# Kernel optimization log

Measured on AMD Instinct MI355X. Metric: run time of the kernel, lower is better.

## Reference

```python
import jax, jax.numpy as jnp
import numpy as np

J = 16384
D = 2048

def setup_inputs() -> dict:
    key = jax.random.key(0)
    embeddings = jax.random.normal(key, (J, D), dtype=jnp.float32)
    return {"embeddings": embeddings}

def reference(embeddings) -> jnp.ndarray:
    J_, d = embeddings.shape
    # position indices j=1..J, feature indices k=1..d (as in the torch loop)
    j = jnp.arange(1, J_ + 1, dtype=embeddings.dtype)  # [J]
    k = jnp.arange(1, d + 1, dtype=embeddings.dtype)   # [d]
    a = 1.0 - j / J_            # [J]
    b = 1.0 - 2.0 * j / J_      # [J]
    # L[j,k] = (1 - j/J) - (k/d)*(1 - 2j/J)
    L = a[:, None] - (k / d)[None, :] * b[:, None]  # [J, d]
    return jnp.sum(L * embeddings, axis=0)  # [d]
```

## Files before the change

kernel.cpp:

```cpp
#include <hip/hip_runtime.h>


constexpr int D_COLS = 2048;
constexpr int J_ROWS = 16384;
constexpr int T1 = 512;
constexpr int B1_MAX = 512;

__global__ __launch_bounds__(T1) void pe_stage1(const float* __restrict__ E,
                                                float* __restrict__ ws,
                                                int nb) {
    const int tid  = threadIdx.x;
    const int col0 = tid * 4;
    const float invJ = 1.0f / (float)J_ROWS;
    const float invD = 1.0f / (float)D_COLS;
    const float c0 = (float)(col0 + 1) * invD;
    const float c1 = (float)(col0 + 2) * invD;
    const float c2 = (float)(col0 + 3) * invD;
    const float c3 = (float)(col0 + 4) * invD;

    float4 acc = make_float4(0.f, 0.f, 0.f, 0.f);
    for (int row = blockIdx.x; row < J_ROWS; row += nb) {
        const float jf = (float)(row + 1);
        const float a = fmaf(-jf,        invJ, 1.0f);
        const float b = fmaf(-2.0f * jf, invJ, 1.0f);
        const float4 e = *reinterpret_cast<const float4*>(E + (size_t)row * D_COLS + col0);
        acc.x = fmaf(fmaf(-c0, b, a), e.x, acc.x);
        acc.y = fmaf(fmaf(-c1, b, a), e.y, acc.y);
        acc.z = fmaf(fmaf(-c2, b, a), e.z, acc.z);
        acc.w = fmaf(fmaf(-c3, b, a), e.w, acc.w);
    }
    *reinterpret_cast<float4*>(ws + (size_t)blockIdx.x * D_COLS + col0) = acc;
}

__global__ __launch_bounds__(256) void pe_stage2(const float* __restrict__ ws,
                                                 float* __restrict__ out,
                                                 int nb) {
    const int k = blockIdx.x * 256 + threadIdx.x;
    if (k >= D_COLS) return;
    float s0 = 0.f, s1 = 0.f, s2 = 0.f, s3 = 0.f;
    int b = 0;
    for (; b + 3 < nb; b += 4) {
        s0 += ws[(size_t)(b + 0) * D_COLS + k];
        s1 += ws[(size_t)(b + 1) * D_COLS + k];
        s2 += ws[(size_t)(b + 2) * D_COLS + k];
        s3 += ws[(size_t)(b + 3) * D_COLS + k];
    }
    for (; b < nb; ++b) s0 += ws[(size_t)b * D_COLS + k];
    out[k] = (s0 + s1) + (s2 + s3);
}

extern "C" void kernel_launch(void* const* d_in, const int* in_sizes, int n_in,
                              void* d_out, int out_size, void* d_ws, size_t ws_size,
                              hipStream_t stream) {
    const float* E = (const float*)d_in[0];
    float* out = (float*)d_out;
    float* ws = (float*)d_ws;

    int nb = B1_MAX;
    const size_t per_block = (size_t)D_COLS * sizeof(float);
    if (ws_size < (size_t)nb * per_block) {
        nb = (int)(ws_size / per_block);
        if (nb < 1) nb = 1;
    }

    pe_stage1<<<nb, T1, 0, stream>>>(E, ws, nb);
    pe_stage2<<<(D_COLS + 255) / 256, 256, 0, stream>>>(ws, out, nb);
}
```

Measured before the change: 225.8 us.

## Replace two-stage reduction with atomic accumulation and unroll row loop by two

The workspace write plus second reduction kernel is replaced by float atomicAdd of each block's partial sums straight into the output, with a small zeroing kernel launched first. The row loop now issues two independent row loads per iteration to raise memory-level parallelism. This removes the 4 MB workspace round trip and the stage-2 pass, at the cost of contended atomics (512 per column) and a summation order that varies from run to run.

```diff
diff --git a/kernel.cpp b/kernel.cpp
--- a/kernel.cpp
+++ b/kernel.cpp
@@ -4,11 +4,15 @@
 constexpr int D_COLS = 2048;
 constexpr int J_ROWS = 16384;
 constexpr int T1 = 512;
-constexpr int B1_MAX = 512;
+constexpr int NB = 512;
 
-__global__ __launch_bounds__(T1) void pe_stage1(const float* __restrict__ E,
-                                                float* __restrict__ ws,
-                                                int nb) {
+__global__ __launch_bounds__(T1) void pe_zero(float* __restrict__ out) {
+    *reinterpret_cast<float4*>(out + threadIdx.x * 4) =
+        make_float4(0.f, 0.f, 0.f, 0.f);
+}
+
+__global__ __launch_bounds__(T1) void pe_fused(const float* __restrict__ E,
+                                               float* __restrict__ out) {
     const int tid  = threadIdx.x;
     const int col0 = tid * 4;
     const float invJ = 1.0f / (float)J_ROWS;
@@ -19,34 +23,33 @@
     const float c3 = (float)(col0 + 4) * invD;
 
     float4 acc = make_float4(0.f, 0.f, 0.f, 0.f);
-    for (int row = blockIdx.x; row < J_ROWS; row += nb) {
-        const float jf = (float)(row + 1);
-        const float a = fmaf(-jf,        invJ, 1.0f);
-        const float b = fmaf(-2.0f * jf, invJ, 1.0f);
-        const float4 e = *reinterpret_cast<const float4*>(E + (size_t)row * D_COLS + col0);
-        acc.x = fmaf(fmaf(-c0, b, a), e.x, acc.x);
-        acc.y = fmaf(fmaf(-c1, b, a), e.y, acc.y);
-        acc.z = fmaf(fmaf(-c2, b, a), e.z, acc.z);
-        acc.w = fmaf(fmaf(-c3, b, a), e.w, acc.w);
+    for (int row = blockIdx.x; row < J_ROWS; row += 2 * NB) {
+        const int r0 = row;
+        const int r1 = row + NB;
+        const float4 e0 = *reinterpret_cast<const float4*>(E + (size_t)r0 * D_COLS + col0);
+        const float4 e1 = *reinterpret_cast<const float4*>(E + (size_t)r1 * D_COLS + col0);
+
+        const float j0 = (float)(r0 + 1);
+        const float a0 = fmaf(-j0,        invJ, 1.0f);
+        const float b0 = fmaf(-2.0f * j0, invJ, 1.0f);
+        const float j1 = (float)(r1 + 1);
+        const float a1 = fmaf(-j1,        invJ, 1.0f);
+        const float b1 = fmaf(-2.0f * j1, invJ, 1.0f);
+
+        acc.x = fmaf(fmaf(-c0, b0, a0), e0.x, acc.x);
+        acc.y = fmaf(fmaf(-c1, b0, a0), e0.y, acc.y);
+        acc.z = fmaf(fmaf(-c2, b0, a0), e0.z, acc.z);
+        acc.w = fmaf(fmaf(-c3, b0, a0), e0.w, acc.w);
+        acc.x = fmaf(fmaf(-c0, b1, a1), e1.x, acc.x);
+        acc.y = fmaf(fmaf(-c1, b1, a1), e1.y, acc.y);
+        acc.z = fmaf(fmaf(-c2, b1, a1), e1.z, acc.z);
+        acc.w = fmaf(fmaf(-c3, b1, a1), e1.w, acc.w);
     }
-    *reinterpret_cast<float4*>(ws + (size_t)blockIdx.x * D_COLS + col0) = acc;
-}
 
-__global__ __launch_bounds__(256) void pe_stage2(const float* __restrict__ ws,
-                                                 float* __restrict__ out,
-                                                 int nb) {
-    const int k = blockIdx.x * 256 + threadIdx.x;
-    if (k >= D_COLS) return;
-    float s0 = 0.f, s1 = 0.f, s2 = 0.f, s3 = 0.f;
-    int b = 0;
-    for (; b + 3 < nb; b += 4) {
-        s0 += ws[(size_t)(b + 0) * D_COLS + k];
-        s1 += ws[(size_t)(b + 1) * D_COLS + k];
-        s2 += ws[(size_t)(b + 2) * D_COLS + k];
-        s3 += ws[(size_t)(b + 3) * D_COLS + k];
-    }
-    for (; b < nb; ++b) s0 += ws[(size_t)b * D_COLS + k];
-    out[k] = (s0 + s1) + (s2 + s3);
+    atomicAdd(out + col0 + 0, acc.x);
+    atomicAdd(out + col0 + 1, acc.y);
+    atomicAdd(out + col0 + 2, acc.z);
+    atomicAdd(out + col0 + 3, acc.w);
 }
 
 extern "C" void kernel_launch(void* const* d_in, const int* in_sizes, int n_in,
@@ -54,15 +57,8 @@
                               hipStream_t stream) {
     const float* E = (const float*)d_in[0];
     float* out = (float*)d_out;
-    float* ws = (float*)d_ws;
+    (void)d_ws; (void)ws_size; (void)in_sizes; (void)n_in; (void)out_size;
 
-    int nb = B1_MAX;
-    const size_t per_block = (size_t)D_COLS * sizeof(float);
-    if (ws_size < (size_t)nb * per_block) {
-        nb = (int)(ws_size / per_block);
-        if (nb < 1) nb = 1;
-    }
-
-    pe_stage1<<<nb, T1, 0, stream>>>(E, ws, nb);
-    pe_stage2<<<(D_COLS + 255) / 256, 256, 0, stream>>>(ws, out, nb);
+    pe_zero<<<1, T1, 0, stream>>>(out);
+    pe_fused<<<NB, T1, 0, stream>>>(E, out);
 }
```

Result: slower. 233.9 us (+3.6%).
